# Kernel optimization log

Measured on AMD Instinct MI355X. Metric: run time of the kernel, lower is better.

Reference implementation:

```python
import jax, jax.numpy as jnp
import numpy as np

K_NEIGHBORS = 32
BN_EPS = 1e-5


def setup_inputs() -> dict:
    key = jax.random.key(0)
    ks = jax.random.split(key, 5)
    B, N, C, OUT = 16, 2048, 3, 32
    x = jax.random.normal(ks[0], (B, N, C), dtype=jnp.float32)
    W1 = jax.random.normal(ks[1], (2 * C, 2 * C), dtype=jnp.float32) * 0.3
    b1 = jax.random.normal(ks[2], (2 * C,), dtype=jnp.float32) * 0.05
    W2 = jax.random.normal(ks[3], (2 * C, OUT), dtype=jnp.float32) * 0.3
    b2 = jax.random.normal(ks[4], (OUT,), dtype=jnp.float32) * 0.05
    return {
        "x": x,
        "W1": W1, "b1": b1,
        "gamma1": jnp.ones((2 * C,), jnp.float32), "beta1": jnp.zeros((2 * C,), jnp.float32),
        "W2": W2, "b2": b2,
        "gamma2": jnp.ones((OUT,), jnp.float32), "beta2": jnp.zeros((OUT,), jnp.float32),
    }


def _batchnorm_train(h, gamma, beta):
    # normalize over all axes except the last (channel) axis, biased variance
    axes = tuple(range(h.ndim - 1))
    mean = jnp.mean(h, axis=axes)
    var = jnp.var(h, axis=axes)
    return gamma * (h - mean) * jax.lax.rsqrt(var + BN_EPS) + beta


def reference(x, W1, b1, gamma1, beta1, W2, b2, gamma2, beta2):
    B, N, C = x.shape
    K = min(K_NEIGHBORS, N)
    # brute-force KNN: squared euclidean distances [B,N,N]
    sq = jnp.sum(x * x, axis=-1)
    d = sq[:, :, None] + sq[:, None, :] - 2.0 * jnp.einsum('bnc,bmc->bnm', x, x)
    _, idx = jax.lax.top_k(-d, K)  # [B,N,K] nearest (self first)
    # gather neighbor points: [B,N,K,C]
    knn = jax.vmap(lambda pts, i: pts[i])(x, idx)
    diffs = x[:, :, None, :] - knn
    h = jnp.concatenate([jnp.broadcast_to(x[:, :, None, :], (B, N, K, C)), diffs], axis=-1)  # [B,N,K,2C]
    h = jax.nn.elu(_batchnorm_train(h @ W1 + b1, gamma1, beta1))
    h = jnp.max(h, axis=2)  # max-pool over K neighbors -> [B,N,2C]
    y = jax.nn.elu(_batchnorm_train(h @ W2 + b2, gamma2, beta2))
    return y
```

## Files before the change

kernel.cpp:

```cpp
#include <hip/hip_runtime.h>
#include <math.h>

namespace {
constexpr int NB = 16, NP = 2048, KNN = 32, CH1 = 6, CH2 = 32;
constexpr int QPB = 8;
constexpr int NBLK = NB * NP / QPB;
constexpr float BN_EPS = 1e-5f;

constexpr size_t OFF_S1REP   = 0;
constexpr size_t OFF_STATS2L = 768;
constexpr size_t OFF_SC1     = 1664;
constexpr size_t OFF_P       = 2048;
constexpr size_t OFF_MINQ    = OFF_P + sizeof(float)*NB*NP*CH1;
}

typedef __attribute__((ext_vector_type(2))) float f32x2;

__device__ __forceinline__ f32x2 pk_mul(f32x2 a, f32x2 b) {
  f32x2 d; asm("v_pk_mul_f32 %0, %1, %2" : "=v"(d) : "v"(a), "v"(b)); return d;
}
__device__ __forceinline__ f32x2 pk_add(f32x2 a, f32x2 b) {
  f32x2 d; asm("v_pk_add_f32 %0, %1, %2" : "=v"(d) : "v"(a), "v"(b)); return d;
}

template <int C> __device__ __forceinline__ int dpp0i(int x) {
  return __builtin_amdgcn_update_dpp(0, x, C, 0xf, 0xf, true);
}
template <int C> __device__ __forceinline__ float dpp0f(float x) {
  return __uint_as_float((unsigned)__builtin_amdgcn_update_dpp(
      0, (int)__float_as_uint(x), C, 0xf, 0xf, true));
}
template <int C> __device__ __forceinline__ float dppInff(float x) {
  return __uint_as_float((unsigned)__builtin_amdgcn_update_dpp(
      0x7F800000, (int)__float_as_uint(x), C, 0xf, 0xf, false));
}
__device__ __forceinline__ int wave_isum_bcast(int x) {
  x += dpp0i<0x111>(x); x += dpp0i<0x112>(x); x += dpp0i<0x114>(x);
  x += dpp0i<0x118>(x); x += dpp0i<0x142>(x); x += dpp0i<0x143>(x);
  return __builtin_amdgcn_readlane(x, 63);
}
__device__ __forceinline__ float wave_fsum63(float x) {
  x += dpp0f<0x111>(x); x += dpp0f<0x112>(x); x += dpp0f<0x114>(x);
  x += dpp0f<0x118>(x); x += dpp0f<0x142>(x); x += dpp0f<0x143>(x);
  return x;
}
__device__ __forceinline__ float wave_fmin63(float x) {
  x = fminf(x, dppInff<0x111>(x)); x = fminf(x, dppInff<0x112>(x));
  x = fminf(x, dppInff<0x114>(x)); x = fminf(x, dppInff<0x118>(x));
  x = fminf(x, dppInff<0x142>(x)); x = fminf(x, dppInff<0x143>(x));
  return x;
}

#define BSEL(m, x, y) ((((x)) & (m)) | (((y)) & ~(m)))

#define RROUND(alive, below, rem, ca, plane)                  \
  { unsigned z_ = BSEL((plane), 0u, (alive));                 \
    int c_ = wave_isum_bcast(__popc(z_));                     \
    if (c_ >= (rem)) { alive = z_; ca = c_; }                 \
    else { rem -= c_; below |= z_; alive &= (plane); ca -= c_; } }

#define RPAIR(alive, below, rem, ca, p0, p1)                                   \
  { unsigned a0_  = BSEL((p0), 0u, (alive));                                   \
    unsigned a1_  = (alive) & (p0);                                            \
    unsigned z00_ = BSEL((p1), 0u, a0_);                                       \
    unsigned z01_ = a0_ & (p1);                                                \
    unsigned z10_ = BSEL((p1), 0u, a1_);                                       \
    unsigned z11_ = a1_ & (p1);                                                \
    int c00_ = wave_isum_bcast(__popc(z00_));                                  \
    int c01_ = wave_isum_bcast(__popc(z01_));                                  \
    int c10_ = wave_isum_bcast(__popc(z10_));                                  \
    if (c00_ >= (rem)) { alive = z00_; ca = c00_; }                            \
    else if (c00_ + c01_ >= (rem)) {                                           \
      below |= z00_; rem -= c00_; alive = z01_; ca = c01_;                     \
    } else if (c00_ + c01_ + c10_ >= (rem)) {                                  \
      below |= z00_ | z01_; rem -= c00_ + c01_; alive = z10_; ca = c10_;       \
    } else {                                                                   \
      below |= z00_ | z01_ | z10_; rem -= c00_ + c01_ + c10_;                  \
      alive = z11_; ca = (ca) - c00_ - c01_ - c10_;                            \
    } }

#define TR16(a)                                                      \
  _Pragma("unroll") for (int g_ = 0; g_ < 8; ++g_) {                 \
    unsigned hi_ = a[g_], lo_ = a[g_+8];                             \
    a[g_]   = __builtin_amdgcn_perm(hi_, lo_, 0x07030501u);          \
    a[g_+8] = __builtin_amdgcn_perm(hi_, lo_, 0x06020400u); }        \
  _Pragma("unroll") for (int g_ = 0; g_ < 8; ++g_) {                 \
    int k_ = (g_ >> 2)*8 + (g_ & 3);                                 \
    unsigned A_ = a[k_], B_ = a[k_+4];                               \
    a[k_]   = BSEL(0x0F0F0F0Fu, B_ >> 4, A_);                        \
    a[k_+4] = BSEL(0xF0F0F0F0u, A_ << 4, B_); }                      \
  _Pragma("unroll") for (int g_ = 0; g_ < 8; ++g_) {                 \
    int k_ = (g_ >> 1)*4 + (g_ & 1);                                 \
    unsigned A_ = a[k_], B_ = a[k_+2];                               \
    a[k_]   = BSEL(0x33333333u, B_ >> 2, A_);                        \
    a[k_+2] = BSEL(0xCCCCCCCCu, A_ << 2, B_); }                      \
  _Pragma("unroll") for (int g_ = 0; g_ < 8; ++g_) {                 \
    int k_ = g_*2;                                                   \
    unsigned A_ = a[k_], B_ = a[k_+1];                               \
    a[k_]   = BSEL(0x55555555u, B_ >> 1, A_);                        \
    a[k_+1] = BSEL(0xAAAAAAAAu, A_ << 1, B_); }

__global__ __launch_bounds__(512, 8) void knn_kernel(const float* __restrict__ x,
                                                     const float* __restrict__ W1,
                                                     const float* __restrict__ b1,
                                                     float* __restrict__ pout,
                                                     float* __restrict__ minq,
                                                     double* __restrict__ s1rep) {
  __shared__ float4 XC[512], YC[512], ZC[512], WC[512];
  __shared__ float red[12][QPB];
  const int lane = threadIdx.x & 63;
  const int w    = threadIdx.x >> 6;
  const int qi   = blockIdx.x * QPB + w;
  const int b    = qi >> 11;
  const int n    = qi & (NP - 1);

  const float* xb = x + (size_t)b * NP * 3;
  {
    const int t = threadIdx.x;
    const int g0 = t >> 6, ls = t & 63;
    float xx[4], yy[4], zz[4], ww[4];
#pragma unroll
    for (int k = 0; k < 4; ++k) {
      const float* pp = xb + (g0*256 + k*64 + ls) * 3;
      float a0 = pp[0], a1 = pp[1], a2 = pp[2];
      xx[k] = a0; yy[k] = a1; zz[k] = a2;
      ww[k] = __fadd_rn(__fadd_rn(__fmul_rn(a0,a0), __fmul_rn(a1,a1)), __fmul_rn(a2,a2));
    }
    XC[t] = (float4){xx[0], xx[1], xx[2], xx[3]};
    YC[t] = (float4){yy[0], yy[1], yy[2], yy[3]};
    ZC[t] = (float4){zz[0], zz[1], zz[2], zz[3]};
    WC[t] = (float4){ww[0], ww[1], ww[2], ww[3]};
  }
  __syncthreads();

  const float* Xs = (const float*)XC;
  const float* Ys = (const float*)YC;
  const float* Zs = (const float*)ZC;
  const float* Ws = (const float*)WC;

  const int vq = n >> 6, lq = n & 63;
  const int qidx = (((vq >> 2) << 6) | lq) * 4 + (vq & 3);
  const float qx = Xs[qidx], qy = Ys[qidx], qz = Zs[qidx], qw = Ws[qidx];
  const f32x2 qx2 = {qx,qx}, qy2 = {qy,qy}, qz2 = {qz,qz}, qw2 = {qw,qw};

  unsigned dd[32];
#pragma unroll
  for (int g = 0; g < 8; ++g) {
    const int cs = g*64 + lane;
    float4 X = XC[cs], Y = YC[cs], Z = ZC[cs], Wv = WC[cs];
    f32x2 x01 = {X.x,X.y}, y01 = {Y.x,Y.y}, z01 = {Z.x,Z.y}, w01 = {Wv.x,Wv.y};
    f32x2 x23 = {X.z,X.w}, y23 = {Y.z,Y.w}, z23 = {Z.z,Z.w}, w23 = {Wv.z,Wv.w};
    f32x2 dotA = pk_add(pk_add(pk_mul(qx2,x01), pk_mul(qy2,y01)), pk_mul(qz2,z01));
    f32x2 dotB = pk_add(pk_add(pk_mul(qx2,x23), pk_mul(qy2,y23)), pk_mul(qz2,z23));
    f32x2 ssA = pk_add(qw2, w01), ssB = pk_add(qw2, w23);
    f32x2 dA = pk_add(dotA, dotA), dB = pk_add(dotB, dotB);
    dd[31-(4*g+0)] = __float_as_uint(__fsub_rn(ssA.x, dA.x));
    dd[31-(4*g+1)] = __float_as_uint(__fsub_rn(ssA.y, dA.y));
    dd[31-(4*g+2)] = __float_as_uint(__fsub_rn(ssB.x, dB.x));
    dd[31-(4*g+3)] = __float_as_uint(__fsub_rn(ssB.y, dB.y));
  }

  unsigned h[16], l[16];
#pragma unroll
  for (int g = 0; g < 16; ++g) {
    h[g] = __builtin_amdgcn_perm(dd[g], dd[g+16], 0x07060302u);
    l[g] = __builtin_amdgcn_perm(dd[g], dd[g+16], 0x05040100u);
  }
  TR16(h);

  unsigned alive = 0xFFFFFFFFu, below = 0u;
  int rem = KNN, ca = 2048;
  RPAIR(alive, below, rem, ca, h[1],  h[2]);
  RPAIR(alive, below, rem, ca, h[3],  h[4]);
  RPAIR(alive, below, rem, ca, h[5],  h[6]);
  if (ca != rem) RPAIR(alive, below, rem, ca, h[7],  h[8]);
  if (ca != rem) RPAIR(alive, below, rem, ca, h[9],  h[10]);
  if (ca != rem) RPAIR(alive, below, rem, ca, h[11], h[12]);
  if (ca != rem) RPAIR(alive, below, rem, ca, h[13], h[14]);
  if (ca != rem) RROUND(alive, below, rem, ca, h[15]);

  unsigned sel;
  if (__builtin_expect(ca == rem, 1)) {
    sel = below | alive;
  } else {
    TR16(l);
#pragma unroll
    for (int i = 0; i < 16; ++i) {
      if (ca != rem) RROUND(alive, below, rem, ca, l[i]);
    }
    sel = below;
    if (ca == rem) {
      sel |= alive;
    } else {
      for (int v = 0; v < 32; ++v) {
        if (rem <= 0) break;
        bool mine = (alive >> v) & 1;
        unsigned long long mb = __ballot(mine);
        int c = __popcll(mb);
        if (c <= rem) { if (mine) sel |= 1u << v; rem -= c; }
        else {
          if (mine && (int)__popcll(mb & ((1ull << lane) - 1)) < rem) sel |= 1u << v;
          rem = 0;
        }
      }
    }
  }

  float w3[CH1], w4[CH1], w5[CH1];
#pragma unroll
  for (int c = 0; c < CH1; ++c) { w3[c]=W1[3*CH1+c]; w4[c]=W1[4*CH1+c]; w5[c]=W1[5*CH1+c]; }
  float sq_[CH1], sqq[CH1], mn[CH1];
#pragma unroll
  for (int c = 0; c < CH1; ++c) { sq_[c] = 0.f; sqq[c] = 0.f; mn[c] = INFINITY; }
  unsigned m = sel;
  while (m) {
    int v = __builtin_ctz(m); m &= m - 1;
    int idx = (((v >> 2) << 6) | lane) * 4 + (v & 3);
    float px_ = Xs[idx], py_ = Ys[idx], pz_ = Zs[idx];
#pragma unroll
    for (int c = 0; c < CH1; ++c) {
      float qv = px_*w3[c] + py_*w4[c] + pz_*w5[c];
      sq_[c] += qv; sqq[c] += qv*qv; mn[c] = fminf(mn[c], qv);
    }
  }

  float pv[CH1];
#pragma unroll
  for (int c = 0; c < CH1; ++c) {
    float qv = qx*w3[c] + qy*w4[c] + qz*w5[c];
    pv[c] = b1[c] + qx*W1[c] + qy*W1[CH1+c] + qz*W1[2*CH1+c] + qv;
  }

#pragma unroll
  for (int c = 0; c < CH1; ++c) {
    float s  = wave_fsum63(sq_[c]);
    float s2 = wave_fsum63(sqq[c]);
    float mm = wave_fmin63(mn[c]);
    if (lane == 63) {
      minq[qi*CH1 + c] = mm;
      red[c][w]       = fmaf(32.f, pv[c], -s);
      red[CH1 + c][w] = fmaf(32.f, pv[c]*pv[c], fmaf(-2.f*pv[c], s, s2));
    }
  }
  if (lane == 0) {
#pragma unroll
    for (int c = 0; c < CH1; ++c) pout[qi*CH1 + c] = pv[c];
  }
  __syncthreads();
  if (threadIdx.x < 12) {
    float s = 0.f;
#pragma unroll
    for (int ww2 = 0; ww2 < QPB; ++ww2) s += red[threadIdx.x][ww2];
    atomicAdd(s1rep + (blockIdx.x & 7) * 12 + threadIdx.x, (double)s);
  }
}

__global__ __launch_bounds__(256) void stage2_kernel(const float* __restrict__ p,
                                                     const float* __restrict__ minq,
                                                     const double* __restrict__ s1rep,
                                                     const float* __restrict__ gamma1,
                                                     const float* __restrict__ beta1,
                                                     float* __restrict__ sc1g,
                                                     double* __restrict__ stats2L) {
  __shared__ double tot1[12];
  __shared__ float sc1s[12];
  __shared__ float acc[4][27];
  const int t = threadIdx.x;
  if (t < 12) {
    double s = 0.0;
#pragma unroll
    for (int r = 0; r < 8; ++r) s += s1rep[r*12 + t];
    tot1[t] = s;
  }
  __syncthreads();
  if (t < CH1) {
    double cnt  = (double)NB * NP * KNN;
    double mean = tot1[t] / cnt;
    double var  = tot1[CH1 + t] / cnt - mean * mean;
    float scale = gamma1[t] / sqrtf((float)var + BN_EPS);
    sc1s[t] = scale; sc1s[CH1 + t] = beta1[t] - (float)mean * scale;
  }
  __syncthreads();
  if (blockIdx.x == 0 && t < 12) sc1g[t] = sc1s[t];

  const int qi = blockIdx.x * 256 + t;
  const int w = t >> 6, lane = t & 63;
  float me[CH1];
#pragma unroll
  for (int c = 0; c < CH1; ++c) {
    float v = fmaf(sc1s[c], p[qi*CH1 + c] - minq[qi*CH1 + c], sc1s[CH1 + c]);
    me[c] = v > 0.f ? v : expm1f(v);
  }
  float vals[27];
#pragma unroll
  for (int c = 0; c < CH1; ++c) vals[c] = me[c];
  {
    int id = 6;
#pragma unroll
    for (int c = 0; c < CH1; ++c)
#pragma unroll
      for (int d = c; d < CH1; ++d) { vals[id] = me[c]*me[d]; ++id; }
  }
#pragma unroll
  for (int k = 0; k < 27; ++k) {
    float s = wave_fsum63(vals[k]);
    if (lane == 63) acc[w][k] = s;
  }
  __syncthreads();
  if (t < 27)
    atomicAdd(stats2L + (blockIdx.x & 3) * 27 + t,
              (double)((acc[0][t] + acc[1][t]) + (acc[2][t] + acc[3][t])));
}

__global__ __launch_bounds__(256) void out_kernel(const float* __restrict__ p,
                                                  const float* __restrict__ minq,
                                                  const float* __restrict__ sc1,
                                                  const float* __restrict__ W2,
                                                  const float* __restrict__ b2,
                                                  const double* __restrict__ stats2L,
                                                  const float* __restrict__ gamma2,
                                                  const float* __restrict__ beta2,
                                                  float* __restrict__ out) {
  __shared__ float m2[27];
  __shared__ float me_lds[8][CH1];
  __shared__ float s2s[CH2], s2h[CH2];
  const int t = threadIdx.x;
  if (t < 27)
    m2[t] = (float)(((stats2L[t] + stats2L[27+t]) + (stats2L[54+t] + stats2L[81+t])));
  const int qbase = blockIdx.x * 8;
  if (t >= 64 && t < 112) {
    int qs = (t - 64) / 6, c = (t - 64) % 6;
    int qi = qbase + qs;
    float v = fmaf(sc1[c], p[qi*CH1 + c] - minq[qi*CH1 + c], sc1[CH1 + c]);
    me_lds[qs][c] = v > 0.f ? v : expm1f(v);
  }
  __syncthreads();
  if (t < CH2) {
    float wv[CH1];
#pragma unroll
    for (int c = 0; c < CH1; ++c) wv[c] = W2[c*CH2 + t];
    float sy = 0.f;
#pragma unroll
    for (int c = 0; c < CH1; ++c) sy = fmaf(wv[c], m2[c], sy);
    float sy2 = 0.f;
    {
      int id = 6;
#pragma unroll
      for (int c = 0; c < CH1; ++c)
#pragma unroll
        for (int d = c; d < CH1; ++d) {
          float coef = (c == d) ? wv[c]*wv[c] : 2.f*wv[c]*wv[d];
          sy2 = fmaf(coef, m2[id], sy2); ++id;
        }
    }
    const double N = (double)NB * NP;
    double bo   = (double)b2[t];
    double mean = ((double)sy + N*bo) / N;
    double Ey2  = ((double)sy2 + 2.0*bo*(double)sy + N*bo*bo) / N;
    double var  = Ey2 - mean*mean;
    float scale = gamma2[t] / sqrtf((float)var + BN_EPS);
    s2s[t] = scale; s2h[t] = beta2[t] - (float)mean * scale;
  }
  __syncthreads();
  const int qs = t >> 5, o = t & 31;
  const int qi = qbase + qs;
  float y = b2[o];
#pragma unroll
  for (int c = 0; c < CH1; ++c) y = fmaf(me_lds[qs][c], W2[c*CH2 + o], y);
  float r = fmaf(s2s[o], y, s2h[o]);
  out[(size_t)qi*CH2 + o] = r > 0.f ? r : expm1f(r);
}

extern "C" void kernel_launch(void* const* d_in, const int* in_sizes, int n_in,
                              void* d_out, int out_size, void* d_ws, size_t ws_size,
                              hipStream_t stream) {
  const float* x      = (const float*)d_in[0];
  const float* W1     = (const float*)d_in[1];
  const float* b1     = (const float*)d_in[2];
  const float* gamma1 = (const float*)d_in[3];
  const float* beta1  = (const float*)d_in[4];
  const float* W2     = (const float*)d_in[5];
  const float* b2     = (const float*)d_in[6];
  const float* gamma2 = (const float*)d_in[7];
  const float* beta2  = (const float*)d_in[8];
  float* out = (float*)d_out;
  char* ws = (char*)d_ws;

  double* s1rep   = (double*)(ws + OFF_S1REP);
  double* stats2L = (double*)(ws + OFF_STATS2L);
  float* sc1  = (float*)(ws + OFF_SC1);
  float* p    = (float*)(ws + OFF_P);
  float* minq = (float*)(ws + OFF_MINQ);

  hipMemsetAsync(ws, 0, 1664, stream);

  knn_kernel   <<<dim3(NBLK),       dim3(512), 0, stream>>>(x, W1, b1, p, minq, s1rep);
  stage2_kernel<<<dim3(NB*NP/256),  dim3(256), 0, stream>>>(p, minq, s1rep, gamma1, beta1,
                                                            sc1, stats2L);
  out_kernel   <<<dim3(NB*NP/8),    dim3(256), 0, stream>>>(p, minq, sc1, W2, b2,
                                                            stats2L, gamma2, beta2, out);
}
```

Baseline: 83.52 us.

## Use compiler vector ops for distances, pack per-neighbor math, relax launch bounds

Replaces the inline-asm packed multiply/add with plain f32x2 vector expressions under contract(off), so the compiler can schedule them freely while keeping bit-exact distance ordering. The per-neighbor W1 projection loop now runs on channel pairs packed into f32x2 so it can use packed FP32 ops. The radix-select guard branches are merged two rounds per check, and launch bounds drop from 8 to 6 waves per SIMD to allow more registers. In exchange it may lower occupancy and relies on the compiler to emit packed instructions.

```diff
diff --git a/kernel.cpp b/kernel.cpp
--- a/kernel.cpp
+++ b/kernel.cpp
@@ -15,13 +15,6 @@
 }
 
 typedef __attribute__((ext_vector_type(2))) float f32x2;
-
-__device__ __forceinline__ f32x2 pk_mul(f32x2 a, f32x2 b) {
-  f32x2 d; asm("v_pk_mul_f32 %0, %1, %2" : "=v"(d) : "v"(a), "v"(b)); return d;
-}
-__device__ __forceinline__ f32x2 pk_add(f32x2 a, f32x2 b) {
-  f32x2 d; asm("v_pk_add_f32 %0, %1, %2" : "=v"(d) : "v"(a), "v"(b)); return d;
-}
 
 template <int C> __device__ __forceinline__ int dpp0i(int x) {
   return __builtin_amdgcn_update_dpp(0, x, C, 0xf, 0xf, true);
@@ -100,7 +93,19 @@
     a[k_]   = BSEL(0x55555555u, B_ >> 1, A_);                        \
     a[k_+1] = BSEL(0xAAAAAAAAu, A_ << 1, B_); }
 
-__global__ __launch_bounds__(512, 8) void knn_kernel(const float* __restrict__ x,
+__device__ __forceinline__ void dist4(f32x2& r01, f32x2& r23,
+                                      f32x2 qx2, f32x2 qy2, f32x2 qz2, f32x2 qw2,
+                                      float4 X, float4 Y, float4 Z, float4 Wv) {
+#pragma clang fp contract(off)
+  f32x2 x01 = {X.x, X.y}, y01 = {Y.x, Y.y}, z01 = {Z.x, Z.y}, w01 = {Wv.x, Wv.y};
+  f32x2 x23 = {X.z, X.w}, y23 = {Y.z, Y.w}, z23 = {Z.z, Z.w}, w23 = {Wv.z, Wv.w};
+  f32x2 dot0 = (qx2 * x01 + qy2 * y01) + qz2 * z01;
+  f32x2 dot1 = (qx2 * x23 + qy2 * y23) + qz2 * z23;
+  r01 = (qw2 + w01) - (dot0 + dot0);
+  r23 = (qw2 + w23) - (dot1 + dot1);
+}
+
+__global__ __launch_bounds__(512, 6) void knn_kernel(const float* __restrict__ x,
                                                      const float* __restrict__ W1,
                                                      const float* __restrict__ b1,
                                                      float* __restrict__ pout,
@@ -147,17 +152,12 @@
 #pragma unroll
   for (int g = 0; g < 8; ++g) {
     const int cs = g*64 + lane;
-    float4 X = XC[cs], Y = YC[cs], Z = ZC[cs], Wv = WC[cs];
-    f32x2 x01 = {X.x,X.y}, y01 = {Y.x,Y.y}, z01 = {Z.x,Z.y}, w01 = {Wv.x,Wv.y};
-    f32x2 x23 = {X.z,X.w}, y23 = {Y.z,Y.w}, z23 = {Z.z,Z.w}, w23 = {Wv.z,Wv.w};
-    f32x2 dotA = pk_add(pk_add(pk_mul(qx2,x01), pk_mul(qy2,y01)), pk_mul(qz2,z01));
-    f32x2 dotB = pk_add(pk_add(pk_mul(qx2,x23), pk_mul(qy2,y23)), pk_mul(qz2,z23));
-    f32x2 ssA = pk_add(qw2, w01), ssB = pk_add(qw2, w23);
-    f32x2 dA = pk_add(dotA, dotA), dB = pk_add(dotB, dotB);
-    dd[31-(4*g+0)] = __float_as_uint(__fsub_rn(ssA.x, dA.x));
-    dd[31-(4*g+1)] = __float_as_uint(__fsub_rn(ssA.y, dA.y));
-    dd[31-(4*g+2)] = __float_as_uint(__fsub_rn(ssB.x, dB.x));
-    dd[31-(4*g+3)] = __float_as_uint(__fsub_rn(ssB.y, dB.y));
+    f32x2 r01, r23;
+    dist4(r01, r23, qx2, qy2, qz2, qw2, XC[cs], YC[cs], ZC[cs], WC[cs]);
+    dd[31-(4*g+0)] = __float_as_uint(r01.x);
+    dd[31-(4*g+1)] = __float_as_uint(r01.y);
+    dd[31-(4*g+2)] = __float_as_uint(r23.x);
+    dd[31-(4*g+3)] = __float_as_uint(r23.y);
   }
 
   unsigned h[16], l[16];
@@ -173,10 +173,14 @@
   RPAIR(alive, below, rem, ca, h[1],  h[2]);
   RPAIR(alive, below, rem, ca, h[3],  h[4]);
   RPAIR(alive, below, rem, ca, h[5],  h[6]);
-  if (ca != rem) RPAIR(alive, below, rem, ca, h[7],  h[8]);
-  if (ca != rem) RPAIR(alive, below, rem, ca, h[9],  h[10]);
-  if (ca != rem) RPAIR(alive, below, rem, ca, h[11], h[12]);
-  if (ca != rem) RPAIR(alive, below, rem, ca, h[13], h[14]);
+  if (ca != rem) {
+    RPAIR(alive, below, rem, ca, h[7],  h[8]);
+    RPAIR(alive, below, rem, ca, h[9],  h[10]);
+  }
+  if (ca != rem) {
+    RPAIR(alive, below, rem, ca, h[11], h[12]);
+    RPAIR(alive, below, rem, ca, h[13], h[14]);
+  }
   if (ca != rem) RROUND(alive, below, rem, ca, h[15]);
 
   unsigned sel;
@@ -206,36 +210,53 @@
     }
   }
 
-  float w3[CH1], w4[CH1], w5[CH1];
-#pragma unroll
-  for (int c = 0; c < CH1; ++c) { w3[c]=W1[3*CH1+c]; w4[c]=W1[4*CH1+c]; w5[c]=W1[5*CH1+c]; }
-  float sq_[CH1], sqq[CH1], mn[CH1];
-#pragma unroll
-  for (int c = 0; c < CH1; ++c) { sq_[c] = 0.f; sqq[c] = 0.f; mn[c] = INFINITY; }
+  f32x2 w3p[3], w4p[3], w5p[3];
+#pragma unroll
+  for (int j = 0; j < 3; ++j) {
+    w3p[j] = (f32x2){W1[3*CH1 + 2*j], W1[3*CH1 + 2*j + 1]};
+    w4p[j] = (f32x2){W1[4*CH1 + 2*j], W1[4*CH1 + 2*j + 1]};
+    w5p[j] = (f32x2){W1[5*CH1 + 2*j], W1[5*CH1 + 2*j + 1]};
+  }
+  f32x2 sqp[3], sqqp[3], mnp[3];
+#pragma unroll
+  for (int j = 0; j < 3; ++j) {
+    sqp[j] = (f32x2){0.f, 0.f}; sqqp[j] = (f32x2){0.f, 0.f};
+    mnp[j] = (f32x2){INFINITY, INFINITY};
+  }
   unsigned m = sel;
   while (m) {
     int v = __builtin_ctz(m); m &= m - 1;
     int idx = (((v >> 2) << 6) | lane) * 4 + (v & 3);
     float px_ = Xs[idx], py_ = Ys[idx], pz_ = Zs[idx];
-#pragma unroll
-    for (int c = 0; c < CH1; ++c) {
-      float qv = px_*w3[c] + py_*w4[c] + pz_*w5[c];
-      sq_[c] += qv; sqq[c] += qv*qv; mn[c] = fminf(mn[c], qv);
+    f32x2 pxp = {px_, px_}, pyp = {py_, py_}, pzp = {pz_, pz_};
+#pragma unroll
+    for (int j = 0; j < 3; ++j) {
+      f32x2 qv = pxp*w3p[j] + pyp*w4p[j] + pzp*w5p[j];
+      sqp[j]  += qv;
+      sqqp[j] += qv*qv;
+      mnp[j].x = fminf(mnp[j].x, qv.x);
+      mnp[j].y = fminf(mnp[j].y, qv.y);
     }
   }
 
   float pv[CH1];
 #pragma unroll
   for (int c = 0; c < CH1; ++c) {
-    float qv = qx*w3[c] + qy*w4[c] + qz*w5[c];
+    float w3c = ((c & 1) ? w3p[c>>1].y : w3p[c>>1].x);
+    float w4c = ((c & 1) ? w4p[c>>1].y : w4p[c>>1].x);
+    float w5c = ((c & 1) ? w5p[c>>1].y : w5p[c>>1].x);
+    float qv = qx*w3c + qy*w4c + qz*w5c;
     pv[c] = b1[c] + qx*W1[c] + qy*W1[CH1+c] + qz*W1[2*CH1+c] + qv;
   }
 
 #pragma unroll
   for (int c = 0; c < CH1; ++c) {
-    float s  = wave_fsum63(sq_[c]);
-    float s2 = wave_fsum63(sqq[c]);
-    float mm = wave_fmin63(mn[c]);
+    float sc  = (c & 1) ? sqp[c>>1].y  : sqp[c>>1].x;
+    float s2c = (c & 1) ? sqqp[c>>1].y : sqqp[c>>1].x;
+    float mc  = (c & 1) ? mnp[c>>1].y  : mnp[c>>1].x;
+    float s  = wave_fsum63(sc);
+    float s2 = wave_fsum63(s2c);
+    float mm = wave_fmin63(mc);
     if (lane == 63) {
       minq[qi*CH1 + c] = mm;
       red[c][w]       = fmaf(32.f, pv[c], -s);
```

Measured after the change: 75.71 us. -9.4%, faster.
